# Optimization experiments

Measured on AMD Instinct MI355X. Metric: run time of the kernel, lower is better.

## Reference

```python
import jax, jax.numpy as jnp
import numpy as np

EMBED = 2048
HEADS = 16
HEAD_DIM = EMBED // HEADS
CHUNK = 128
BASE = 10000.0
EPS = 1e-6


def setup_inputs() -> dict:
    key = jax.random.key(0)
    ks = jax.random.split(key, 8)
    b, n, d = 2, 2048, EMBED
    std = 0.02
    return {
        "x": jax.random.normal(ks[0], (b, n, d), jnp.float32),
        "Wq": jax.random.normal(ks[1], (d, d), jnp.float32) * std,
        "Wk": jax.random.normal(ks[2], (d, d), jnp.float32) * std,
        "Wv": jax.random.normal(ks[3], (d, d), jnp.float32) * std,
        "Wo": jax.random.normal(ks[4], (d, d), jnp.float32) * std,
        "Wg1": jax.random.normal(ks[5], (d, HEAD_DIM), jnp.float32) * std,
        "Wg2": jax.random.normal(ks[6], (HEAD_DIM, d), jnp.float32) * std,
        "norm_weight": jnp.ones((d,), jnp.float32),
    }


def _alibi_log_decay(h):
    # lightning attention 'constant' decay: per-head ALiBi slope, log_lambda = -slope
    slopes = 2.0 ** (-8.0 * (jnp.arange(h, dtype=jnp.float32) + 1.0) / h)
    return -slopes  # [h]


def _lrpe_rotate(x):
    # RoPE-like rotation on head_dim (half-split), offset=0
    b, n, h, d = x.shape
    half = d // 2
    theta = BASE ** (-2.0 * jnp.arange(half, dtype=jnp.float32) / d)  # [half]
    ang = jnp.arange(n, dtype=jnp.float32)[:, None] * theta[None, :]  # [n, half]
    cos = jnp.cos(ang)[None, :, None, :]
    sin = jnp.sin(ang)[None, :, None, :]
    x1, x2 = x[..., :half], x[..., half:]
    return jnp.concatenate([x1 * cos - x2 * sin, x1 * sin + x2 * cos], axis=-1)


def _lightning_attn(q, k, v, log_lam):
    # chunk-recurrent linear attention with per-head exponential decay
    b, n, h, d = q.shape
    C = CHUNK
    nc = n // C
    qc = q.reshape(b, nc, C, h, d).transpose(1, 0, 2, 3, 4)  # [nc,b,C,h,d]
    kc = k.reshape(b, nc, C, h, d).transpose(1, 0, 2, 3, 4)
    vc = v.reshape(b, nc, C, h, d).transpose(1, 0, 2, 3, 4)
    i = jnp.arange(C, dtype=jnp.float32)
    diff = i[:, None] - i[None, :]  # [C,C]
    # intra-chunk decay mask D[h,t,s] = lambda_h^(t-s) for t>=s else 0
    D = jnp.where(diff[None] >= 0, jnp.exp(log_lam[:, None, None] * diff[None]), 0.0)
    decay_q = jnp.exp(log_lam[None, :] * (i[:, None] + 1.0))    # [C,h]
    decay_k = jnp.exp(log_lam[None, :] * (C - 1.0 - i[:, None]))  # [C,h]
    lam_C = jnp.exp(log_lam * C)  # [h]

    def step(S, qkv):
        qi, ki, vi = qkv  # [b,C,h,d]
        scores = jnp.einsum('bthd,bshd->bhts', qi, ki) * D[None]
        o_intra = jnp.einsum('bhts,bshd->bthd', scores, vi)
        o_inter = jnp.einsum('bthd,bhde->bthe', qi * decay_q[None, :, :, None], S)
        S_new = lam_C[None, :, None, None] * S + jnp.einsum(
            'bshd,bshe->bhde', ki * decay_k[None, :, :, None], vi)
        return S_new, o_intra + o_inter

    S0 = jnp.zeros((b, h, d, d), q.dtype)
    _, o = jax.lax.scan(step, S0, (qc, kc, vc))  # o: [nc,b,C,h,d]
    return o.transpose(1, 0, 2, 3, 4).reshape(b, n, h, d)


def _gated_group_rmsnorm(o, gate, weight):
    # gate_pos='pre', gate_act='sigmoid', num_groups=HEADS
    b, n, d = o.shape
    x = o * jax.nn.sigmoid(gate)
    xg = x.reshape(b, n, HEADS, HEAD_DIM)
    ms = jnp.mean(xg * xg, axis=-1, keepdims=True)
    xg = xg * jax.lax.rsqrt(ms + EPS)
    return xg.reshape(b, n, d) * weight


def reference(x, Wq, Wk, Wv, Wo, Wg1, Wg2, norm_weight):
    b, n, d = x.shape
    q = (x @ Wq).reshape(b, n, HEADS, HEAD_DIM)
    k = (x @ Wk).reshape(b, n, HEADS, HEAD_DIM)
    v = (x @ Wv).reshape(b, n, HEADS, HEAD_DIM)
    q = jax.nn.silu(q)
    k = jax.nn.silu(k)
    q = _lrpe_rotate(q)
    k = _lrpe_rotate(k)
    log_lam = _alibi_log_decay(HEADS)
    o = _lightning_attn(q, k, v, log_lam).reshape(b, n, d)
    gate = (x @ Wg1) @ Wg2
    o = _gated_group_rmsnorm(o, gate, norm_weight)
    return o @ Wo
```

## Files before the change

kernel.cpp:

```cpp
#include <hip/hip_runtime.h>


#define DEV __device__ __forceinline__
typedef unsigned short u16;
typedef __bf16 bf16x8 __attribute__((ext_vector_type(8)));
typedef float f32x4 __attribute__((ext_vector_type(4)));
typedef u16 u16x8 __attribute__((ext_vector_type(8)));

DEV u16 f2bf(float f) {
  unsigned u = __builtin_bit_cast(unsigned, f);
  u += 0x7fffu + ((u >> 16) & 1u);
  return (u16)(u >> 16);
}
DEV float bf2f(u16 h) {
  unsigned u = ((unsigned)h) << 16;
  return __builtin_bit_cast(float, u);
}
DEV void async16(const u16* g, u16* l) {
  __builtin_amdgcn_global_load_lds(
      (const __attribute__((address_space(1))) unsigned int*)g,
      (__attribute__((address_space(3))) unsigned int*)l, 16, 0, 0);
}

__global__ void convert_f32_bf16(const float* __restrict__ in, u16* __restrict__ out, long n) {
  long i = ((long)blockIdx.x * blockDim.x + threadIdx.x) * 4;
  if (i >= n) return;
  float4 v = *(const float4*)(in + i);
  ushort4 p;
  p.x = f2bf(v.x); p.y = f2bf(v.y); p.z = f2bf(v.z); p.w = f2bf(v.w);
  *(ushort4*)(out + i) = p;
}

__global__ void transpose_all(const float* __restrict__ Wq, const float* __restrict__ Wk,
                              const float* __restrict__ Wv, const float* __restrict__ Wo,
                              const float* __restrict__ Wg1, const float* __restrict__ Wg2,
                              u16* __restrict__ wtqkvg, u16* __restrict__ wot,
                              u16* __restrict__ wg2t) {
  __shared__ float t[32][33];
  int id = blockIdx.x;
  const float* in; u16* out; int K, N, bx, by;
  bool perm = false;
  if (id < 12288) {
    int w = id >> 12, tt = id & 4095;
    in = (w == 0) ? Wq : (w == 1) ? Wk : Wv;
    out = wtqkvg + (long)w * 2048 * 2048;
    K = 2048; N = 2048; bx = tt & 63; by = tt >> 6;
    perm = (w < 2);
  } else if (id < 16384) {
    int tt = id - 12288;
    in = Wo; out = wot; K = 2048; N = 2048; bx = tt & 63; by = tt >> 6;
  } else if (id < 16640) {
    int tt = id - 16384;
    in = Wg1; out = wtqkvg + 6144L * 2048; K = 2048; N = 128; bx = tt & 3; by = tt >> 2;
  } else {
    int tt = id - 16640;
    in = Wg2; out = wg2t; K = 128; N = 2048; bx = tt & 63; by = tt >> 6;
  }
  int c = threadIdx.x & 31, r0 = threadIdx.x >> 5;
  for (int r = r0; r < 32; r += 8)
    t[r][c] = in[(long)(by * 32 + r) * N + bx * 32 + c];
  __syncthreads();
  for (int r = r0; r < 32; r += 8) {
    int n = bx * 32 + r, nr = n;
    if (perm) {
      int h = n >> 7, j = n & 127, jj = j & 63, hi = j >> 6;
      nr = h * 128 + (jj & 15) + 32 * (jj >> 4) + 16 * hi;
    }
    out[(long)nr * K + by * 32 + c] = f2bf(t[c][r]);
  }
}

template <typename OutT>
__global__ __launch_bounds__(256, 2) void gemm_bt(
    const u16* __restrict__ A, const u16* __restrict__ B, OutT* __restrict__ C,
    int M, int N, int K, int lda, int ldb, int ldc, int rot,
    int nc, long sA1, long sA2, long sB1, long sB2, long sC1, long sC2) {
  __shared__ u16 sA[128 * 32], sB[128 * 32];
  {
    int z = blockIdx.z, z1 = z / nc, z2 = z % nc;
    A += z1 * sA1 + z2 * sA2;
    B += z1 * sB1 + z2 * sB2;
    C += z1 * sC1 + z2 * sC2;
  }
  int bxs, bys;
  {
    int lin = blockIdx.x + gridDim.x * blockIdx.y;
    int per = 16 * gridDim.y;
    int g = lin / per, r = lin % per;
    int base = g * 16;
    int w = min(16, (int)gridDim.x - base);
    bxs = base + r % w; bys = r / w;
  }
  const int tid = threadIdx.x, lane = tid & 63, wid = tid >> 6;
  const int bm = bys * 128, bn = bxs * 128;
  const int ch0 = wid * 2, ch1 = ch0 + 1;
  const int lr = lane >> 2;
  const int ak = (((lane & 3) - ((lane >> 3) & 3)) & 3) * 8;
  const int ar0 = ch0 * 16 + lr, ar1 = ch1 * 16 + lr;
  const u16* gA0 = A + (long)(bm + ar0) * lda + ak;
  const u16* gA1 = A + (long)(bm + ar1) * lda + ak;
  const u16* gB0 = B + (long)(bn + ar0) * ldb + ak;
  const u16* gB1 = B + (long)(bn + ar1) * ldb + ak;
  u16* lA0 = sA + ch0 * 512; u16* lA1 = sA + ch1 * 512;
  u16* lB0 = sB + ch0 * 512; u16* lB1 = sB + ch1 * 512;
  const int wm = (wid & 1) * 64, wn = (wid >> 1) * 64;
  const int fm = lane & 15, kq = lane >> 4;
  const int qs = ((kq + (fm >> 1)) & 3) * 8;
  const int aoff = (wm >> 4) * 512 + fm * 32 + qs;
  const int boff = (wn >> 4) * 512 + fm * 32 + qs;
  f32x4 acc[4][4] = {};
  for (int kb = 0; kb < K; kb += 32) {
    async16(gA0, lA0); async16(gA1, lA1);
    async16(gB0, lB0); async16(gB1, lB1);
    gA0 += 32; gA1 += 32; gB0 += 32; gB1 += 32;
    __syncthreads();
    bf16x8 af[4], bfr[4];
#pragma unroll
    for (int i = 0; i < 4; i++) af[i] = *(const bf16x8*)&sA[aoff + i * 512];
#pragma unroll
    for (int i = 0; i < 4; i++) bfr[i] = *(const bf16x8*)&sB[boff + i * 512];
#pragma unroll
    for (int mt = 0; mt < 4; mt++)
#pragma unroll
      for (int nt = 0; nt < 4; nt++)
        acc[mt][nt] = __builtin_amdgcn_mfma_f32_16x16x32_bf16(af[mt], bfr[nt], acc[mt][nt], 0, 0, 0);
    __syncthreads();
  }
  const int cr = (lane >> 4) * 4;
  if constexpr (sizeof(OutT) == 2) {
    if (rot == 1 && bn < 4096) {
#pragma unroll
      for (int mt = 0; mt < 4; mt++)
#pragma unroll
        for (int r = 0; r < 4; r++) {
          long row = bm + wm + mt * 16 + cr + r;
          float tf = (float)(int)(row & 2047);
#pragma unroll
          for (int np = 0; np < 4; np += 2) {
            float x1 = acc[mt][np][r], x2 = acc[mt][np + 1][r];
            x1 = x1 / (1.f + __expf(-x1));
            x2 = x2 / (1.f + __expf(-x2));
            int jj = fm + 16 * ((wn >> 5) + (np >> 1));
            float th = exp2f(-13.287712379549449f * (float)jj * (1.f / 64.f));
            float sn, cs;
            sincosf(tf * th, &sn, &cs);
            C[row * ldc + bn + jj]      = f2bf(x1 * cs - x2 * sn);
            C[row * ldc + bn + 64 + jj] = f2bf(x1 * sn + x2 * cs);
          }
        }
      return;
    }
  }
#pragma unroll
  for (int mt = 0; mt < 4; mt++)
#pragma unroll
    for (int nt = 0; nt < 4; nt++)
#pragma unroll
      for (int r = 0; r < 4; r++) {
        long row = bm + wm + mt * 16 + cr + r;
        long col = bn + wn + nt * 16 + fm;
        float v = acc[mt][nt][r];
        if constexpr (sizeof(OutT) == 2) {
          if (rot == 2) v = 1.f / (1.f + __expf(-v));
          C[row * ldc + col] = f2bf(v);
        } else {
          C[row * ldc + col] = v;
        }
      }
}

__global__ void transpose_kv(const u16* __restrict__ qkv, u16* __restrict__ kdT,
                             u16* __restrict__ vT) {
  __shared__ float t[32][33];
  int z = blockIdx.z, which = z >> 5, bh = z & 31;
  int b = bh >> 4, h = bh & 15;
  u16* out = which ? vT : kdT;
  int slab = which ? 2 : 1, decay = which ? 0 : 1;
  int n0 = blockIdx.x * 32, d0 = blockIdx.y * 32;
  int cc = threadIdx.x & 31, rr0 = threadIdx.x >> 5;
  float log_lam = -exp2f(-0.5f * (float)(h + 1));
  for (int rr = rr0; rr < 32; rr += 8) {
    int n = n0 + rr;
    float v = bf2f(qkv[(long)(b * 2048 + n) * 6272 + slab * 2048 + h * 128 + d0 + cc]);
    if (decay) v *= expf(log_lam * (float)(127 - (n & 127)));
    t[rr][cc] = v;
  }
  __syncthreads();
  for (int rr = rr0; rr < 32; rr += 8)
    out[((long)bh * 128 + d0 + rr) * 2048 + n0 + cc] = f2bf(t[cc][rr]);
}

__global__ void scan_state(const u16* __restrict__ U, u16* __restrict__ S_all) {
  int blk = blockIdx.x;
  int bh = blk >> 3, sl = blk & 7, h = bh & 15;
  float log_lam = -exp2f(-0.5f * (float)(h + 1));
  float lamC = expf(log_lam * 128.f);
  long off = (long)bh * 16 * 16384 + sl * 2048 + threadIdx.x * 8;
  float s[8];
#pragma unroll
  for (int j = 0; j < 8; j++) s[j] = 0.f;
  for (int c = 0; c < 16; c++) {
    long idx = off + (long)c * 16384;
    u16x8 sb;
#pragma unroll
    for (int j = 0; j < 8; j++) sb[j] = f2bf(s[j]);
    *(u16x8*)(S_all + idx) = sb;
    u16x8 ub = *(const u16x8*)(U + idx);
#pragma unroll
    for (int j = 0; j < 8; j++) s[j] = lamC * s[j] + bf2f(ub[j]);
  }
}

__global__ __launch_bounds__(256, 2) void attn_out(
    const u16* __restrict__ qkv, const u16* __restrict__ vT,
    const u16* __restrict__ S_all, const u16* __restrict__ gate,
    const float* __restrict__ nw, u16* __restrict__ nrm) {
  __shared__ u16 sA[128 * 32], sB[128 * 32], sK[128 * 32];
  __shared__ u16 sS[128 * 136];
  __shared__ float sNorm[2][128];
  const int blk = blockIdx.x;
  const int bh = blk >> 4, c = blk & 15;
  const int b = bh >> 4, h = bh & 15;
  const float log_lam = -exp2f(-0.5f * (float)(h + 1));
  const int tid = threadIdx.x, lane = tid & 63, wid = tid >> 6;
  const int wm = (wid & 1) * 64, wn = (wid >> 1) * 64;
  const int fm = lane & 15, fq = lane >> 4, kq = lane >> 4;
  const int lr = lane >> 2;
  const int ak = (((lane & 3) - ((lane >> 3) & 3)) & 3) * 8;
  const int ch0 = wid * 2, ch1 = ch0 + 1;
  const int r0 = ch0 * 16 + lr, r1 = ch1 * 16 + lr;
  const int qs = ((kq + (fm >> 1)) & 3) * 8;
  const int aoff = (wm >> 4) * 512 + fm * 32 + qs;
  const int boff = (wn >> 4) * 512 + fm * 32 + qs;
  const u16* qbase = qkv + (long)(b * 2048 + c * 128) * 6272 + h * 128;
  const u16* kbase = qbase + 2048;
  const u16* Sbase = S_all + ((long)bh * 16 + c) * 16384;
  const u16* vbase = vT + (long)bh * 262144 + (long)c * 128;

  f32x4 acc[4][4] = {};
  f32x4 sc[4][4] = {};
  for (int kb = 0; kb < 128; kb += 32) {
    async16(qbase + (long)r0 * 6272 + kb + ak, sA + ch0 * 512);
    async16(qbase + (long)r1 * 6272 + kb + ak, sA + ch1 * 512);
    async16(Sbase + r0 * 128 + kb + ak, sB + ch0 * 512);
    async16(Sbase + r1 * 128 + kb + ak, sB + ch1 * 512);
    async16(kbase + (long)r0 * 6272 + kb + ak, sK + ch0 * 512);
    async16(kbase + (long)r1 * 6272 + kb + ak, sK + ch1 * 512);
    __syncthreads();
    bf16x8 aq[4], bs[4], bk[4];
#pragma unroll
    for (int i = 0; i < 4; i++) {
      aq[i] = *(const bf16x8*)&sA[aoff + i * 512];
      bs[i] = *(const bf16x8*)&sB[boff + i * 512];
      bk[i] = *(const bf16x8*)&sK[boff + i * 512];
    }
#pragma unroll
    for (int mt = 0; mt < 4; mt++)
#pragma unroll
      for (int nt = 0; nt < 4; nt++) {
        acc[mt][nt] = __builtin_amdgcn_mfma_f32_16x16x32_bf16(aq[mt], bs[nt], acc[mt][nt], 0, 0, 0);
        sc[mt][nt] = __builtin_amdgcn_mfma_f32_16x16x32_bf16(aq[mt], bk[nt], sc[mt][nt], 0, 0, 0);
      }
    __syncthreads();
  }
#pragma unroll
  for (int mt = 0; mt < 4; mt++)
#pragma unroll
    for (int r = 0; r < 4; r++) {
      int t = wm + mt * 16 + fq * 4 + r;
      float d = __expf(log_lam * (float)(t + 1));
#pragma unroll
      for (int nt = 0; nt < 4; nt++) acc[mt][nt][r] *= d;
    }
  float eS[4];
#pragma unroll
  for (int nt = 0; nt < 4; nt++)
    eS[nt] = __expf(log_lam * (float)(63 - (nt * 16 + fm)));
#pragma unroll
  for (int mt = 0; mt < 4; mt++)
#pragma unroll
    for (int r = 0; r < 4; r++) {
      int t = wm + mt * 16 + fq * 4 + r;
      float eT = __expf(log_lam * (float)(t - wn - 63));
#pragma unroll
      for (int nt = 0; nt < 4; nt++) {
        int s = wn + nt * 16 + fm;
        float v = sc[mt][nt][r];
        v = (t >= s) ? v * (eT * eS[nt]) : 0.f;
        sS[t * 136 + s] = f2bf(v);
      }
    }
  __syncthreads();
  for (int kb = 0; kb < 128; kb += 32) {
    async16(vbase + r0 * 2048 + kb + ak, sB + ch0 * 512);
    async16(vbase + r1 * 2048 + kb + ak, sB + ch1 * 512);
    __syncthreads();
    bf16x8 as[4], bv[4];
#pragma unroll
    for (int i = 0; i < 4; i++) {
      as[i] = *(const bf16x8*)&sS[(wm + i * 16 + fm) * 136 + kb + kq * 8];
      bv[i] = *(const bf16x8*)&sB[boff + i * 512];
    }
#pragma unroll
    for (int mt = 0; mt < 4; mt++)
#pragma unroll
      for (int nt = 0; nt < 4; nt++)
        acc[mt][nt] = __builtin_amdgcn_mfma_f32_16x16x32_bf16(as[mt], bv[nt], acc[mt][nt], 0, 0, 0);
    __syncthreads();
  }
  const u16* gbase = gate + (long)(b * 2048 + c * 128) * 2048 + h * 128;
  float nwv[4];
#pragma unroll
  for (int nt = 0; nt < 4; nt++) nwv[nt] = nw[h * 128 + wn + nt * 16 + fm];
  float part[4][4];
#pragma unroll
  for (int mt = 0; mt < 4; mt++)
#pragma unroll
    for (int r = 0; r < 4; r++) {
      int t = wm + mt * 16 + fq * 4 + r;
      float p = 0.f;
#pragma unroll
      for (int nt = 0; nt < 4; nt++) {
        int e = wn + nt * 16 + fm;
        float g = bf2f(gbase[(long)t * 2048 + e]);
        float x = acc[mt][nt][r] * g;
        acc[mt][nt][r] = x;
        p += x * x;
      }
      part[mt][r] = p;
    }
#pragma unroll
  for (int o = 1; o < 16; o <<= 1)
#pragma unroll
    for (int mt = 0; mt < 4; mt++)
#pragma unroll
      for (int r = 0; r < 4; r++) part[mt][r] += __shfl_xor(part[mt][r], o);
  if (fm == 0) {
#pragma unroll
    for (int mt = 0; mt < 4; mt++)
#pragma unroll
      for (int r = 0; r < 4; r++)
        sNorm[wid >> 1][wm + mt * 16 + fq * 4 + r] = part[mt][r];
  }
  __syncthreads();
  long orow0 = (long)(b * 2048 + c * 128);
#pragma unroll
  for (int mt = 0; mt < 4; mt++)
#pragma unroll
    for (int r = 0; r < 4; r++) {
      int t = wm + mt * 16 + fq * 4 + r;
      float ms = (sNorm[0][t] + sNorm[1][t]) * (1.f / 128.f);
      float rs = rsqrtf(ms + 1e-6f);
#pragma unroll
      for (int nt = 0; nt < 4; nt++) {
        int e = wn + nt * 16 + fm;
        nrm[(orow0 + t) * 2048 + h * 128 + e] = f2bf(acc[mt][nt][r] * rs * nwv[nt]);
      }
    }
}

extern "C" void kernel_launch(void* const* d_in, const int* in_sizes, int n_in,
                              void* d_out, int out_size, void* d_ws, size_t ws_size,
                              hipStream_t stream) {
  (void)in_sizes; (void)n_in; (void)out_size; (void)ws_size;
  const float* x   = (const float*)d_in[0];
  const float* Wq  = (const float*)d_in[1];
  const float* Wk  = (const float*)d_in[2];
  const float* Wv  = (const float*)d_in[3];
  const float* Wo  = (const float*)d_in[4];
  const float* Wg1 = (const float*)d_in[5];
  const float* Wg2 = (const float*)d_in[6];
  const float* nw  = (const float*)d_in[7];
  float* out = (float*)d_out;

  char* ws = (char*)d_ws;
  size_t off = 0;
  auto alloc = [&](size_t bytes) -> void* {
    void* p = ws + off;
    off += (bytes + 255) & ~(size_t)255;
    return p;
  };
  u16* xb    = (u16*)alloc(4096UL * 2048 * 2);
  u16* wtqkv = (u16*)alloc(6272UL * 2048 * 2);
  u16* wot   = (u16*)alloc(2048UL * 2048 * 2);
  u16* wg2t  = (u16*)alloc(2048UL * 128 * 2);
  u16* qkvg  = (u16*)alloc(4096UL * 6272 * 2);
  u16* gate  = (u16*)alloc(4096UL * 2048 * 2);
  u16* kdT   = (u16*)alloc(32UL * 128 * 2048 * 2);
  u16* vT    = (u16*)alloc(32UL * 128 * 2048 * 2);
  u16* Ubuf  = (u16*)alloc(512UL * 16384 * 2);
  u16* S_all = (u16*)alloc(512UL * 16384 * 2);
  u16* nrm   = (u16*)alloc(4096UL * 2048 * 2);

  convert_f32_bf16<<<dim3(8192), dim3(256), 0, stream>>>(x, xb, 8388608L);
  transpose_all<<<dim3(16896), dim3(256), 0, stream>>>(Wq, Wk, Wv, Wo, Wg1, Wg2,
                                                       wtqkv, wot, wg2t);
  gemm_bt<u16><<<dim3(49, 32, 1), dim3(256), 0, stream>>>(xb, wtqkv, qkvg,
      4096, 6272, 2048, 2048, 2048, 6272, 1, 1, 0, 0, 0, 0, 0, 0);
  gemm_bt<u16><<<dim3(16, 32, 1), dim3(256), 0, stream>>>(qkvg + 6144, wg2t, gate,
      4096, 2048, 128, 6272, 128, 2048, 2, 1, 0, 0, 0, 0, 0, 0);
  transpose_kv<<<dim3(64, 4, 64), dim3(256), 0, stream>>>(qkvg, kdT, vT);
  gemm_bt<u16><<<dim3(1, 1, 512), dim3(256), 0, stream>>>(vT, kdT, Ubuf,
      128, 128, 128, 2048, 2048, 128, 0,
      16, 262144L, 128L, 262144L, 128L, 262144L, 16384L);
  scan_state<<<dim3(256), dim3(256), 0, stream>>>(Ubuf, S_all);
  attn_out<<<dim3(512), dim3(256), 0, stream>>>(qkvg, vT, S_all, gate, nw, nrm);
  gemm_bt<float><<<dim3(16, 32, 1), dim3(256), 0, stream>>>(nrm, wot, out,
      4096, 2048, 2048, 2048, 2048, 2048, 0, 1, 0, 0, 0, 0, 0, 0);
}
```

Measured before the change: 408.9 us.

## Fuse prep kernels, precompute RoPE table, write V transposed from QKV GEMM epilogue

Merges the x conversion and weight transposes into one prep kernel, which also fills a cos/sin table for the rotary embedding. The QKV GEMM epilogue now reads that table instead of calling sincosf per element. The same epilogue writes the V columns straight into the transposed vT layout, so the transpose pass only handles K. This removes a launch, per-element transcendentals and half of the transpose traffic, at the cost of a table lookup and strided 8-byte stores in the GEMM epilogue.

```diff
diff --git a/kernel.cpp b/kernel.cpp
--- a/kernel.cpp
+++ b/kernel.cpp
@@ -6,6 +6,7 @@
 typedef __bf16 bf16x8 __attribute__((ext_vector_type(8)));
 typedef float f32x4 __attribute__((ext_vector_type(4)));
 typedef u16 u16x8 __attribute__((ext_vector_type(8)));
+typedef u16 u16x4 __attribute__((ext_vector_type(4)));
 
 DEV u16 f2bf(float f) {
   unsigned u = __builtin_bit_cast(unsigned, f);
@@ -22,22 +23,33 @@
       (__attribute__((address_space(3))) unsigned int*)l, 16, 0, 0);
 }
 
-__global__ void convert_f32_bf16(const float* __restrict__ in, u16* __restrict__ out, long n) {
-  long i = ((long)blockIdx.x * blockDim.x + threadIdx.x) * 4;
-  if (i >= n) return;
-  float4 v = *(const float4*)(in + i);
-  ushort4 p;
-  p.x = f2bf(v.x); p.y = f2bf(v.y); p.z = f2bf(v.z); p.w = f2bf(v.w);
-  *(ushort4*)(out + i) = p;
-}
-
-__global__ void transpose_all(const float* __restrict__ Wq, const float* __restrict__ Wk,
-                              const float* __restrict__ Wv, const float* __restrict__ Wo,
-                              const float* __restrict__ Wg1, const float* __restrict__ Wg2,
-                              u16* __restrict__ wtqkvg, u16* __restrict__ wot,
-                              u16* __restrict__ wg2t) {
+__global__ void prep_all(const float* __restrict__ x,
+                         const float* __restrict__ Wq, const float* __restrict__ Wk,
+                         const float* __restrict__ Wv, const float* __restrict__ Wo,
+                         const float* __restrict__ Wg1, const float* __restrict__ Wg2,
+                         u16* __restrict__ xb, u16* __restrict__ wtqkvg,
+                         u16* __restrict__ wot, u16* __restrict__ wg2t,
+                         float* __restrict__ rope) {
+  int id = blockIdx.x;
+  if (id < 8192) {
+    long i = ((long)id * 256 + threadIdx.x) * 4;
+    float4 v = *(const float4*)(x + i);
+    ushort4 p;
+    p.x = f2bf(v.x); p.y = f2bf(v.y); p.z = f2bf(v.z); p.w = f2bf(v.w);
+    *(ushort4*)(xb + i) = p;
+    return;
+  }
+  if (id >= 25088) {
+    int idx = (id - 25088) * 256 + threadIdx.x;
+    int t = idx >> 6, jj = idx & 63;
+    float th = exp2f(-13.287712379549449f * (float)jj * (1.f / 64.f));
+    float sn, cs;
+    sincosf((float)t * th, &sn, &cs);
+    ((float2*)rope)[idx] = make_float2(cs, sn);
+    return;
+  }
+  id -= 8192;
   __shared__ float t[32][33];
-  int id = blockIdx.x;
   const float* in; u16* out; int K, N, bx, by;
   bool perm = false;
   if (id < 12288) {
@@ -74,7 +86,8 @@
 __global__ __launch_bounds__(256, 2) void gemm_bt(
     const u16* __restrict__ A, const u16* __restrict__ B, OutT* __restrict__ C,
     int M, int N, int K, int lda, int ldb, int ldc, int rot,
-    int nc, long sA1, long sA2, long sB1, long sB2, long sC1, long sC2) {
+    int nc, long sA1, long sA2, long sB1, long sB2, long sC1, long sC2,
+    const float* __restrict__ rope, u16* __restrict__ VT) {
   __shared__ u16 sA[128 * 32], sB[128 * 32];
   {
     int z = blockIdx.z, z1 = z / nc, z2 = z % nc;
@@ -134,20 +147,35 @@
 #pragma unroll
         for (int r = 0; r < 4; r++) {
           long row = bm + wm + mt * 16 + cr + r;
-          float tf = (float)(int)(row & 2047);
+          const float2* rp = (const float2*)rope + (long)(row & 2047) * 64;
 #pragma unroll
           for (int np = 0; np < 4; np += 2) {
             float x1 = acc[mt][np][r], x2 = acc[mt][np + 1][r];
             x1 = x1 / (1.f + __expf(-x1));
             x2 = x2 / (1.f + __expf(-x2));
             int jj = fm + 16 * ((wn >> 5) + (np >> 1));
-            float th = exp2f(-13.287712379549449f * (float)jj * (1.f / 64.f));
-            float sn, cs;
-            sincosf(tf * th, &sn, &cs);
-            C[row * ldc + bn + jj]      = f2bf(x1 * cs - x2 * sn);
-            C[row * ldc + bn + 64 + jj] = f2bf(x1 * sn + x2 * cs);
+            float2 cn = rp[jj];
+            C[row * ldc + bn + jj]      = f2bf(x1 * cn.x - x2 * cn.y);
+            C[row * ldc + bn + 64 + jj] = f2bf(x1 * cn.y + x2 * cn.x);
           }
         }
+      return;
+    }
+    if (rot == 1 && bn < 6144) {
+      const int bq = bm >> 11;
+#pragma unroll
+      for (int mt = 0; mt < 4; mt++) {
+        const int t0 = (bm + wm + mt * 16 + cr) & 2047;
+#pragma unroll
+        for (int nt = 0; nt < 4; nt++) {
+          int f = bn - 4096 + wn + nt * 16 + fm;
+          long vrow = (long)(bq * 16 + (f >> 7)) * 128 + (f & 127);
+          u16x4 pk;
+#pragma unroll
+          for (int r = 0; r < 4; r++) pk[r] = f2bf(acc[mt][nt][r]);
+          *(u16x4*)(VT + vrow * 2048 + t0) = pk;
+        }
+      }
       return;
     }
   }
@@ -169,25 +197,22 @@
       }
 }
 
-__global__ void transpose_kv(const u16* __restrict__ qkv, u16* __restrict__ kdT,
-                             u16* __restrict__ vT) {
+__global__ void transpose_k(const u16* __restrict__ qkv, u16* __restrict__ kdT) {
   __shared__ float t[32][33];
-  int z = blockIdx.z, which = z >> 5, bh = z & 31;
+  int bh = blockIdx.z;
   int b = bh >> 4, h = bh & 15;
-  u16* out = which ? vT : kdT;
-  int slab = which ? 2 : 1, decay = which ? 0 : 1;
   int n0 = blockIdx.x * 32, d0 = blockIdx.y * 32;
   int cc = threadIdx.x & 31, rr0 = threadIdx.x >> 5;
   float log_lam = -exp2f(-0.5f * (float)(h + 1));
   for (int rr = rr0; rr < 32; rr += 8) {
     int n = n0 + rr;
-    float v = bf2f(qkv[(long)(b * 2048 + n) * 6272 + slab * 2048 + h * 128 + d0 + cc]);
-    if (decay) v *= expf(log_lam * (float)(127 - (n & 127)));
+    float v = bf2f(qkv[(long)(b * 2048 + n) * 6272 + 2048 + h * 128 + d0 + cc]);
+    v *= expf(log_lam * (float)(127 - (n & 127)));
     t[rr][cc] = v;
   }
   __syncthreads();
   for (int rr = rr0; rr < 32; rr += 8)
-    out[((long)bh * 128 + d0 + rr) * 2048 + n0 + cc] = f2bf(t[cc][rr]);
+    kdT[((long)bh * 128 + d0 + rr) * 2048 + n0 + cc] = f2bf(t[cc][rr]);
 }
 
 __global__ void scan_state(const u16* __restrict__ U, u16* __restrict__ S_all) {
@@ -391,20 +416,20 @@
   u16* Ubuf  = (u16*)alloc(512UL * 16384 * 2);
   u16* S_all = (u16*)alloc(512UL * 16384 * 2);
   u16* nrm   = (u16*)alloc(4096UL * 2048 * 2);
-
-  convert_f32_bf16<<<dim3(8192), dim3(256), 0, stream>>>(x, xb, 8388608L);
-  transpose_all<<<dim3(16896), dim3(256), 0, stream>>>(Wq, Wk, Wv, Wo, Wg1, Wg2,
-                                                       wtqkv, wot, wg2t);
+  float* rope = (float*)alloc(2048UL * 64 * 8);
+
+  prep_all<<<dim3(25600), dim3(256), 0, stream>>>(x, Wq, Wk, Wv, Wo, Wg1, Wg2,
+                                                  xb, wtqkv, wot, wg2t, rope);
   gemm_bt<u16><<<dim3(49, 32, 1), dim3(256), 0, stream>>>(xb, wtqkv, qkvg,
-      4096, 6272, 2048, 2048, 2048, 6272, 1, 1, 0, 0, 0, 0, 0, 0);
+      4096, 6272, 2048, 2048, 2048, 6272, 1, 1, 0, 0, 0, 0, 0, 0, rope, vT);
   gemm_bt<u16><<<dim3(16, 32, 1), dim3(256), 0, stream>>>(qkvg + 6144, wg2t, gate,
-      4096, 2048, 128, 6272, 128, 2048, 2, 1, 0, 0, 0, 0, 0, 0);
-  transpose_kv<<<dim3(64, 4, 64), dim3(256), 0, stream>>>(qkvg, kdT, vT);
+      4096, 2048, 128, 6272, 128, 2048, 2, 1, 0, 0, 0, 0, 0, 0, nullptr, nullptr);
+  transpose_k<<<dim3(64, 4, 32), dim3(256), 0, stream>>>(qkvg, kdT);
   gemm_bt<u16><<<dim3(1, 1, 512), dim3(256), 0, stream>>>(vT, kdT, Ubuf,
       128, 128, 128, 2048, 2048, 128, 0,
-      16, 262144L, 128L, 262144L, 128L, 262144L, 16384L);
+      16, 262144L, 128L, 262144L, 128L, 262144L, 16384L, nullptr, nullptr);
   scan_state<<<dim3(256), dim3(256), 0, stream>>>(Ubuf, S_all);
   attn_out<<<dim3(512), dim3(256), 0, stream>>>(qkvg, vT, S_all, gate, nw, nrm);
   gemm_bt<float><<<dim3(16, 32, 1), dim3(256), 0, stream>>>(nrm, wot, out,
-      4096, 2048, 2048, 2048, 2048, 2048, 0, 1, 0, 0, 0, 0, 0, 0);
-}
+      4096, 2048, 2048, 2048, 2048, 2048, 0, 1, 0, 0, 0, 0, 0, 0, nullptr, nullptr);
+}
```

Result: no change. 403.0 us (-1.5%).
